# Optimization experiments

Measured on AMD Instinct MI355X. Metric: run time of the kernel, lower is better.

## Reference

```python
import jax, jax.numpy as jnp
import numpy as np

B, N, C, H, W = 16, 10, 128, 48, 48

def setup_inputs() -> dict:
    key = jax.random.key(0)
    k0, k1 = jax.random.split(key, 2)
    x = jax.random.normal(k0, (B, N, C, H, W), dtype=jnp.float32)
    # trainable interpolation params, initialized to 0.5 as in the torch module
    pos_dec = jnp.full((N,), 0.5, dtype=jnp.float32)
    length_dec = jnp.full((N,), 0.5, dtype=jnp.float32)
    # 1x1 conv == channel-mixing matmul over N*C channels
    NC = N * C
    conv_w = jax.random.normal(k1, (NC, NC), dtype=jnp.float32) * (1.0 / np.sqrt(NC))
    conv_b = jnp.zeros((NC,), dtype=jnp.float32)
    return {"x": x, "pos_dec": pos_dec, "length_dec": length_dec,
            "conv_w": conv_w, "conv_b": conv_b}


def reference(x, pos_dec, length_dec, conv_w, conv_b):
    b, n, c, h, w = x.shape
    d = c * h * w
    q = x.reshape(b, n, d)          # proj_query (B,N,CHW)
    k = q                           # proj_key has the same flattened features
    # bi_interpolate with pos_int=i, length_int=1 reduces in closed form to:
    #   s0 = (1-pd)*K[i]   + pd*K[i+1]                      (key_short row)
    #   s1 = ld*((1-pd)*K[i+1] + pd*K[i+2])                 (zero-padded short mixed with key_long)
    # where indices wrap mod N (key was concatenated with itself).
    idx = jnp.arange(n)
    k1_ = k[:, (idx + 1) % n]       # (B,N,D)
    k2_ = k[:, (idx + 2) % n]
    pd = pos_dec[None, :, None]
    ld = length_dec[None, :, None]
    s0 = (1.0 - pd) * k + pd * k1_
    s1 = ld * ((1.0 - pd) * k1_ + pd * k2_)
    S = jnp.stack([s0, s1], axis=2)                 # (B,N,2,D) interpolated keys per group
    logits = jnp.einsum('bnd,bnkd->bnk', q, S)      # per-group 2-way attention scores
    attn = jax.nn.softmax(logits, axis=-1)          # softmax over the 2 searched keys
    out = jnp.einsum('bnk,bnkd->bnd', attn, S)      # (B,N,D)
    feat = out.reshape(b, n * c, h, w)
    conv = jnp.einsum('oc,bchw->bohw', conv_w, feat) + conv_b[None, :, None, None]
    return conv + x.reshape(b, n * c, h, w)
```

## Files before the change

kernel.cpp:

```cpp
#include <hip/hip_runtime.h>
#include <hip/hip_bf16.h>

#define BB 16
#define NN 10
#define CC 128
#define HWD 2304
#define DD (CC*HWD)
#define NC (NN*CC)

#define CH2 72
#define CHUNK2 4096

#define BM 256
#define BN 256
#define BK 64
#define TK (NC/BK)

typedef __bf16 bf16x8 __attribute__((ext_vector_type(8)));
typedef float  f32x4  __attribute__((ext_vector_type(4)));

#define FEAT_BYTES ((size_t)BB*HWD*NC*2)
#define WB_BYTES   ((size_t)NC*NC*2)
#define PART_FLOATS (BB*NN*CH2*3)

__device__ __forceinline__ ushort f2bf(float f) {
    __hip_bfloat16 h = __float2bfloat16(f);
    return *reinterpret_cast<ushort*>(&h);
}

__device__ __forceinline__ void gload_lds16(const ushort* g, ushort* l) {
    __builtin_amdgcn_global_load_lds(
        (const __attribute__((address_space(1))) void*)(const void*)g,
        (__attribute__((address_space(3))) void*)(void*)l,
        16, 0, 0);
}

__global__ __launch_bounds__(256) void k_dots(const float* __restrict__ x,
                                              float* __restrict__ part) {
    int blk = blockIdx.x;
    int ch = blk % CH2;
    int b  = blk / CH2;
    const float* base = x + (size_t)b*NN*DD + (size_t)ch*CHUNK2;
    int t = threadIdx.x;

    float4 cur[4], nxt[4], inc[4];
    #pragma unroll
    for (int i = 0; i < 4; ++i) cur[i] = *(const float4*)(base + (size_t)0*DD + i*1024 + t*4);
    #pragma unroll
    for (int i = 0; i < 4; ++i) nxt[i] = *(const float4*)(base + (size_t)1*DD + i*1024 + t*4);

    __shared__ float red[4][3];
    int w = t >> 6, l = t & 63;

    for (int n = 0; n < NN; ++n) {
        int n2 = (n + 2) % NN;
        #pragma unroll
        for (int i = 0; i < 4; ++i) inc[i] = *(const float4*)(base + (size_t)n2*DD + i*1024 + t*4);

        float s0 = 0.f, s1 = 0.f, s2 = 0.f;
        #pragma unroll
        for (int i = 0; i < 4; ++i) {
            s0 += cur[i].x*cur[i].x + cur[i].y*cur[i].y + cur[i].z*cur[i].z + cur[i].w*cur[i].w;
            s1 += cur[i].x*nxt[i].x + cur[i].y*nxt[i].y + cur[i].z*nxt[i].z + cur[i].w*nxt[i].w;
            s2 += cur[i].x*inc[i].x + cur[i].y*inc[i].y + cur[i].z*inc[i].z + cur[i].w*inc[i].w;
        }
        for (int o = 32; o > 0; o >>= 1) {
            s0 += __shfl_down(s0, o);
            s1 += __shfl_down(s1, o);
            s2 += __shfl_down(s2, o);
        }
        if (l == 0) { red[w][0] = s0; red[w][1] = s1; red[w][2] = s2; }
        __syncthreads();
        if (t == 0) {
            float r0 = 0.f, r1 = 0.f, r2 = 0.f;
            #pragma unroll
            for (int i = 0; i < 4; ++i) { r0 += red[i][0]; r1 += red[i][1]; r2 += red[i][2]; }
            float* o = part + ((size_t)(b*NN + n)*CH2 + ch)*3;
            o[0] = r0; o[1] = r1; o[2] = r2;
        }
        __syncthreads();
        #pragma unroll
        for (int i = 0; i < 4; ++i) { cur[i] = nxt[i]; nxt[i] = inc[i]; }
    }
}

__global__ void k_coef(const float* __restrict__ part,
                       const float* __restrict__ pos_dec,
                       const float* __restrict__ len_dec,
                       float* __restrict__ coef) {
    int bn = threadIdx.x;
    if (bn >= BB*NN) return;
    int n = bn % NN;
    float d0 = 0.f, d1 = 0.f, d2 = 0.f;
    const float* p = part + (size_t)bn*CH2*3;
    for (int i = 0; i < CH2; ++i) { d0 += p[i*3]; d1 += p[i*3+1]; d2 += p[i*3+2]; }
    float pd = pos_dec[n], ld = len_dec[n];
    float l0 = (1.f - pd)*d0 + pd*d1;
    float l1 = ld*((1.f - pd)*d1 + pd*d2);
    float m  = fmaxf(l0, l1);
    float e0 = expf(l0 - m), e1 = expf(l1 - m);
    float inv = 1.f/(e0 + e1);
    float a0 = e0*inv, a1 = e1*inv;
    coef[bn*3+0] = a0*(1.f - pd);
    coef[bn*3+1] = a0*pd + a1*ld*(1.f - pd);
    coef[bn*3+2] = a1*ld*pd;
}

__global__ __launch_bounds__(256) void k_wconv(const float* __restrict__ w,
                                               ushort* __restrict__ wb) {
    int i = blockIdx.x*blockDim.x + threadIdx.x;
    size_t idx = (size_t)i*4;
    if (idx >= (size_t)NC*NC) return;
    float4 a = *(const float4*)(w + idx);
    ushort4 o;
    o.x = f2bf(a.x); o.y = f2bf(a.y); o.z = f2bf(a.z); o.w = f2bf(a.w);
    *(ushort4*)(wb + idx) = o;
}

__global__ __launch_bounds__(256) void k_feat(const float* __restrict__ x,
                                              const float* __restrict__ coef,
                                              ushort* __restrict__ featT) {
    __shared__ float tile[32*129];
    int hwt = blockIdx.x;
    int b   = blockIdx.y;
    int t = threadIdx.x;
    int hw0 = hwt*32;
    const float* xb = x + (size_t)b*NN*DD;

    int c_[4], ch_[4];
    size_t off_[4];
    #pragma unroll
    for (int i = 0; i < 4; ++i) {
        int s = i*256 + t;
        c_[i] = s >> 3; ch_[i] = s & 7;
        off_[i] = (size_t)c_[i]*HWD + hw0 + ch_[i]*4;
    }

    float4 s0[4], s1[4], s2[4], s3[4];
    #pragma unroll
    for (int i = 0; i < 4; ++i) s0[i] = *(const float4*)(xb + (size_t)0*DD + off_[i]);
    #pragma unroll
    for (int i = 0; i < 4; ++i) s1[i] = *(const float4*)(xb + (size_t)1*DD + off_[i]);
    #pragma unroll
    for (int i = 0; i < 4; ++i) s2[i] = *(const float4*)(xb + (size_t)2*DD + off_[i]);

    for (int n = 0; n < NN; ++n) {
        int n3 = (n + 3) % NN;
        #pragma unroll
        for (int i = 0; i < 4; ++i) s3[i] = *(const float4*)(xb + (size_t)n3*DD + off_[i]);

        int bn = b*NN + n;
        float c0 = coef[bn*3+0], c1 = coef[bn*3+1], c2 = coef[bn*3+2];

        #pragma unroll
        for (int i = 0; i < 4; ++i) {
            int hwb = ch_[i]*4, cc = c_[i];
            tile[(hwb+0)*129 + cc] = c0*s0[i].x + c1*s1[i].x + c2*s2[i].x;
            tile[(hwb+1)*129 + cc] = c0*s0[i].y + c1*s1[i].y + c2*s2[i].y;
            tile[(hwb+2)*129 + cc] = c0*s0[i].z + c1*s1[i].z + c2*s2[i].z;
            tile[(hwb+3)*129 + cc] = c0*s0[i].w + c1*s1[i].w + c2*s2[i].w;
        }
        __syncthreads();

        int hwl = t >> 4;
        int cc0 = (t & 15) * 8;
        #pragma unroll
        for (int p = 0; p < 2; ++p) {
            int hw = p*16 + hwl;
            const float* src = &tile[hw*129 + cc0];
            union { ushort us[8]; uint4 v; } pk;
            #pragma unroll
            for (int j = 0; j < 8; ++j) pk.us[j] = f2bf(src[j]);
            ushort* dst = featT + (size_t)b*HWD*NC + (size_t)(hw0 + hw)*NC + n*CC + cc0;
            *(uint4*)dst = pk.v;
        }
        __syncthreads();
        #pragma unroll
        for (int i = 0; i < 4; ++i) { s0[i] = s1[i]; s1[i] = s2[i]; s2[i] = s3[i]; }
    }
}

#define BAR()   __builtin_amdgcn_s_barrier()
#define SB()    __builtin_amdgcn_sched_barrier(0)
#define LGKM0() asm volatile("s_waitcnt lgkmcnt(0)" ::: "memory")
#define VM(N)   asm volatile("s_waitcnt vmcnt(" #N ")" ::: "memory")

__global__ __launch_bounds__(512, 2) void k_gemm(const ushort* __restrict__ Wb,
                                                 const ushort* __restrict__ featT,
                                                 const float* __restrict__ bias,
                                                 const float* __restrict__ x,
                                                 float* __restrict__ out) {
    __shared__ ushort L[2][4][BM*32];

    int bid = blockIdx.x;
    int wkid = (bid & 7) * 90 + (bid >> 3);
    int b   = wkid / 45;
    int r45 = wkid % 45;
    int hwt = r45 / 5;
    int ot  = r45 % 5;
    int o0 = ot*BM, hw0 = hwt*BN;

    int t = threadIdx.x;
    int l = t & 63;
    int w = t >> 6;
    int wr = w >> 2, wc = w & 3;

    const ushort* Ag = Wb + (size_t)o0*NC;
    const ushort* Bg = featT + (size_t)b*HWD*NC + (size_t)hw0*NC;

    int r0 = t >> 2, c0 = t & 3;
    size_t g0 = (size_t)r0*NC + (size_t)((c0 ^ ((r0 >> 1) & 3)) * 8);
    size_t g1 = g0 + (size_t)128*NC;

#define STAGE(nb_, reg_, gp_) do { \
    gload_lds16((gp_) + g0, &L[nb_][reg_][t*8]); \
    gload_lds16((gp_) + g1, &L[nb_][reg_][(512 + t)*8]); } while (0)

    int fr = l & 15;
    int kc = ((l >> 4) ^ ((l >> 1) & 3)) * 8;
    int rowA = (wr*128 + fr)*32 + kc;
    int rowB = (wc*64  + fr)*32 + kc;

    f32x4 acc[8][4] = {};
    bf16x8 af[8], bfA, bfB;

    STAGE(0, 0, Ag);
    STAGE(0, 2, Bg);
    STAGE(0, 1, Ag + 32);
    STAGE(0, 3, Bg + 32);
    VM(4);
    BAR(); SB();

    for (int kt = 0; kt < TK - 1; ++kt) {
        int buf = kt & 1, nbuf = buf ^ 1;
        const ushort* A0 = &L[buf][0][0];
        const ushort* A1 = &L[buf][1][0];
        const ushort* B0 = &L[buf][2][0];
        const ushort* B1 = &L[buf][3][0];
        const ushort* Agk = Ag + (size_t)(kt + 1)*BK;
        const ushort* Bgk = Bg + (size_t)(kt + 1)*BK;

        #pragma unroll
        for (int i = 0; i < 8; ++i) af[i] = *(const bf16x8*)&A0[rowA + i*512];
        bfA = *(const bf16x8*)&B0[rowB];
        bfB = *(const bf16x8*)&B0[rowB + 512];
        STAGE(nbuf, 0, Agk);
        SB(); BAR(); LGKM0(); SB();
        __builtin_amdgcn_s_setprio(1);
        #pragma unroll
        for (int i = 0; i < 8; ++i) {
            acc[i][0] = __builtin_amdgcn_mfma_f32_16x16x32_bf16(af[i], bfA, acc[i][0], 0, 0, 0);
            acc[i][1] = __builtin_amdgcn_mfma_f32_16x16x32_bf16(af[i], bfB, acc[i][1], 0, 0, 0);
        }
        __builtin_amdgcn_s_setprio(0);
        SB(); BAR(); SB();

        bfA = *(const bf16x8*)&B0[rowB + 2*512];
        bfB = *(const bf16x8*)&B0[rowB + 3*512];
        STAGE(nbuf, 2, Bgk);
        SB(); BAR(); LGKM0(); SB();
        __builtin_amdgcn_s_setprio(1);
        #pragma unroll
        for (int i = 0; i < 8; ++i) {
            acc[i][2] = __builtin_amdgcn_mfma_f32_16x16x32_bf16(af[i], bfA, acc[i][2], 0, 0, 0);
            acc[i][3] = __builtin_amdgcn_mfma_f32_16x16x32_bf16(af[i], bfB, acc[i][3], 0, 0, 0);
        }
        __builtin_amdgcn_s_setprio(0);
        SB(); VM(4); BAR(); SB();

        #pragma unroll
        for (int i = 0; i < 8; ++i) af[i] = *(const bf16x8*)&A1[rowA + i*512];
        bfA = *(const bf16x8*)&B1[rowB];
        bfB = *(const bf16x8*)&B1[rowB + 512];
        STAGE(nbuf, 1, Agk + 32);
        SB(); BAR(); LGKM0(); SB();
        __builtin_amdgcn_s_setprio(1);
        #pragma unroll
        for (int i = 0; i < 8; ++i) {
            acc[i][0] = __builtin_amdgcn_mfma_f32_16x16x32_bf16(af[i], bfA, acc[i][0], 0, 0, 0);
            acc[i][1] = __builtin_amdgcn_mfma_f32_16x16x32_bf16(af[i], bfB, acc[i][1], 0, 0, 0);
        }
        __builtin_amdgcn_s_setprio(0);
        SB(); BAR(); SB();

        bfA = *(const bf16x8*)&B1[rowB + 2*512];
        bfB = *(const bf16x8*)&B1[rowB + 3*512];
        STAGE(nbuf, 3, Bgk + 32);
        SB(); BAR(); LGKM0(); SB();
        __builtin_amdgcn_s_setprio(1);
        #pragma unroll
        for (int i = 0; i < 8; ++i) {
            acc[i][2] = __builtin_amdgcn_mfma_f32_16x16x32_bf16(af[i], bfA, acc[i][2], 0, 0, 0);
            acc[i][3] = __builtin_amdgcn_mfma_f32_16x16x32_bf16(af[i], bfB, acc[i][3], 0, 0, 0);
        }
        __builtin_amdgcn_s_setprio(0);
        SB(); VM(4); BAR(); SB();
    }

    {
        const int buf = (TK - 1) & 1;
        const ushort* A0 = &L[buf][0][0];
        const ushort* A1 = &L[buf][1][0];
        const ushort* B0 = &L[buf][2][0];
        const ushort* B1 = &L[buf][3][0];

        #pragma unroll
        for (int i = 0; i < 8; ++i) af[i] = *(const bf16x8*)&A0[rowA + i*512];
        bfA = *(const bf16x8*)&B0[rowB];
        bfB = *(const bf16x8*)&B0[rowB + 512];
        #pragma unroll
        for (int i = 0; i < 8; ++i) {
            acc[i][0] = __builtin_amdgcn_mfma_f32_16x16x32_bf16(af[i], bfA, acc[i][0], 0, 0, 0);
            acc[i][1] = __builtin_amdgcn_mfma_f32_16x16x32_bf16(af[i], bfB, acc[i][1], 0, 0, 0);
        }
        bfA = *(const bf16x8*)&B0[rowB + 2*512];
        bfB = *(const bf16x8*)&B0[rowB + 3*512];
        #pragma unroll
        for (int i = 0; i < 8; ++i) {
            acc[i][2] = __builtin_amdgcn_mfma_f32_16x16x32_bf16(af[i], bfA, acc[i][2], 0, 0, 0);
            acc[i][3] = __builtin_amdgcn_mfma_f32_16x16x32_bf16(af[i], bfB, acc[i][3], 0, 0, 0);
        }
        VM(0);
        BAR(); SB();
        #pragma unroll
        for (int i = 0; i < 8; ++i) af[i] = *(const bf16x8*)&A1[rowA + i*512];
        bfA = *(const bf16x8*)&B1[rowB];
        bfB = *(const bf16x8*)&B1[rowB + 512];
        #pragma unroll
        for (int i = 0; i < 8; ++i) {
            acc[i][0] = __builtin_amdgcn_mfma_f32_16x16x32_bf16(af[i], bfA, acc[i][0], 0, 0, 0);
            acc[i][1] = __builtin_amdgcn_mfma_f32_16x16x32_bf16(af[i], bfB, acc[i][1], 0, 0, 0);
        }
        bfA = *(const bf16x8*)&B1[rowB + 2*512];
        bfB = *(const bf16x8*)&B1[rowB + 3*512];
        #pragma unroll
        for (int i = 0; i < 8; ++i) {
            acc[i][2] = __builtin_amdgcn_mfma_f32_16x16x32_bf16(af[i], bfA, acc[i][2], 0, 0, 0);
            acc[i][3] = __builtin_amdgcn_mfma_f32_16x16x32_bf16(af[i], bfB, acc[i][3], 0, 0, 0);
        }
    }
#undef STAGE

    #pragma unroll
    for (int m = 0; m < 8; ++m) {
        int ro_base = o0 + wr*128 + m*16 + ((l >> 4) << 2);
        #pragma unroll
        for (int n = 0; n < 4; ++n) {
            int col = hw0 + wc*64 + n*16 + (l & 15);
            #pragma unroll
            for (int r = 0; r < 4; ++r) {
                int ro = ro_base + r;
                size_t idx = (size_t)b*NC*HWD + (size_t)ro*HWD + col;
                out[idx] = acc[m][n][r] + bias[ro] + x[idx];
            }
        }
    }
}

extern "C" void kernel_launch(void* const* d_in, const int* in_sizes, int n_in,
                              void* d_out, int out_size, void* d_ws, size_t ws_size,
                              hipStream_t stream) {
    const float* x       = (const float*)d_in[0];
    const float* pos_dec = (const float*)d_in[1];
    const float* len_dec = (const float*)d_in[2];
    const float* conv_w  = (const float*)d_in[3];
    const float* conv_b  = (const float*)d_in[4];
    float* out = (float*)d_out;

    char* ws = (char*)d_ws;
    ushort* featT = (ushort*)ws;
    ushort* wb    = (ushort*)(ws + FEAT_BYTES);
    float*  part  = (float*)(ws + FEAT_BYTES + WB_BYTES);
    float*  coef  = part + PART_FLOATS;

    k_dots <<<dim3(BB*CH2), 256, 0, stream>>>(x, part);
    k_coef <<<dim3(1), 256, 0, stream>>>(part, pos_dec, len_dec, coef);
    k_wconv<<<dim3(1600), 256, 0, stream>>>(conv_w, wb);
    k_feat <<<dim3(72, BB), 256, 0, stream>>>(x, coef, featT);
    k_gemm <<<dim3(720), 512, 0, stream>>>(wb, featT, conv_b, x, out);
}
```

Measured before the change: 300.2 us.

## Fold attention coefficients into per-batch weights and fuse dots with transpose

Rather than building the interpolated feature tensor from x via coefficients, the per-group attention mixing is folded algebraically into a per-batch weight matrix W2[b] = sum of shifted conv_w column blocks scaled by coefficients. The dot-product kernel now also transposes x to bf16 in the same pass, so x is read once for both the dots and the GEMM operand. This removes the separate k_feat pass over x. In exchange it writes a 16x larger weight tensor (per batch, about 52 MB bf16) and requires a large workspace, with a fallback to the old path when the workspace is too small.

Measured after the change: 285.3 us. 1.05x faster.

```diff
diff --git a/kernel.cpp b/kernel.cpp
--- a/kernel.cpp
+++ b/kernel.cpp
@@ -8,8 +8,7 @@
 #define DD (CC*HWD)
 #define NC (NN*CC)
 
-#define CH2 72
-#define CHUNK2 4096
+#define CHP 72
 
 #define BM 256
 #define BN 256
@@ -19,9 +18,11 @@
 typedef __bf16 bf16x8 __attribute__((ext_vector_type(8)));
 typedef float  f32x4  __attribute__((ext_vector_type(4)));
 
-#define FEAT_BYTES ((size_t)BB*HWD*NC*2)
-#define WB_BYTES   ((size_t)NC*NC*2)
-#define PART_FLOATS (BB*NN*CH2*3)
+#define XT_BYTES ((size_t)BB*HWD*NC*2)
+#define W2_BYTES ((size_t)BB*NC*NC*2)
+#define WB_BYTES ((size_t)NC*NC*2)
+#define PART_FLOATS (BB*NN*CHP*3)
+#define HEAD ((size_t)262144)
 
 __device__ __forceinline__ ushort f2bf(float f) {
     __hip_bfloat16 h = __float2bfloat16(f);
@@ -35,52 +36,88 @@
         16, 0, 0);
 }
 
-__global__ __launch_bounds__(256) void k_dots(const float* __restrict__ x,
-                                              float* __restrict__ part) {
-    int blk = blockIdx.x;
-    int ch = blk % CH2;
-    int b  = blk / CH2;
-    const float* base = x + (size_t)b*NN*DD + (size_t)ch*CHUNK2;
+__global__ __launch_bounds__(256) void k_trans(const float* __restrict__ x,
+                                               ushort* __restrict__ xT,
+                                               float* __restrict__ part) {
+    __shared__ float tile[32*129];
+    __shared__ float red[4][3];
+    int hwt = blockIdx.x;
+    int b   = blockIdx.y;
     int t = threadIdx.x;
-
-    float4 cur[4], nxt[4], inc[4];
-    #pragma unroll
-    for (int i = 0; i < 4; ++i) cur[i] = *(const float4*)(base + (size_t)0*DD + i*1024 + t*4);
-    #pragma unroll
-    for (int i = 0; i < 4; ++i) nxt[i] = *(const float4*)(base + (size_t)1*DD + i*1024 + t*4);
-
-    __shared__ float red[4][3];
+    int hw0 = hwt*32;
+    const float* xb = x + (size_t)b*NN*DD;
+
+    int c_[4], ch_[4];
+    size_t off_[4];
+    #pragma unroll
+    for (int i = 0; i < 4; ++i) {
+        int s = i*256 + t;
+        c_[i] = s >> 3; ch_[i] = s & 7;
+        off_[i] = (size_t)c_[i]*HWD + hw0 + ch_[i]*4;
+    }
+
+    float4 s0[4], s1[4], s2[4], s3[4];
+    #pragma unroll
+    for (int i = 0; i < 4; ++i) s0[i] = *(const float4*)(xb + (size_t)0*DD + off_[i]);
+    #pragma unroll
+    for (int i = 0; i < 4; ++i) s1[i] = *(const float4*)(xb + (size_t)1*DD + off_[i]);
+    #pragma unroll
+    for (int i = 0; i < 4; ++i) s2[i] = *(const float4*)(xb + (size_t)2*DD + off_[i]);
+
     int w = t >> 6, l = t & 63;
 
     for (int n = 0; n < NN; ++n) {
-        int n2 = (n + 2) % NN;
-        #pragma unroll
-        for (int i = 0; i < 4; ++i) inc[i] = *(const float4*)(base + (size_t)n2*DD + i*1024 + t*4);
-
-        float s0 = 0.f, s1 = 0.f, s2 = 0.f;
+        int n3 = (n + 3) % NN;
+        #pragma unroll
+        for (int i = 0; i < 4; ++i) s3[i] = *(const float4*)(xb + (size_t)n3*DD + off_[i]);
+
+        float d0 = 0.f, d1 = 0.f, d2 = 0.f;
         #pragma unroll
         for (int i = 0; i < 4; ++i) {
-            s0 += cur[i].x*cur[i].x + cur[i].y*cur[i].y + cur[i].z*cur[i].z + cur[i].w*cur[i].w;
-            s1 += cur[i].x*nxt[i].x + cur[i].y*nxt[i].y + cur[i].z*nxt[i].z + cur[i].w*nxt[i].w;
-            s2 += cur[i].x*inc[i].x + cur[i].y*inc[i].y + cur[i].z*inc[i].z + cur[i].w*inc[i].w;
+            d0 += s0[i].x*s0[i].x + s0[i].y*s0[i].y + s0[i].z*s0[i].z + s0[i].w*s0[i].w;
+            d1 += s0[i].x*s1[i].x + s0[i].y*s1[i].y + s0[i].z*s1[i].z + s0[i].w*s1[i].w;
+            d2 += s0[i].x*s2[i].x + s0[i].y*s2[i].y + s0[i].z*s2[i].z + s0[i].w*s2[i].w;
         }
         for (int o = 32; o > 0; o >>= 1) {
-            s0 += __shfl_down(s0, o);
-            s1 += __shfl_down(s1, o);
-            s2 += __shfl_down(s2, o);
-        }
-        if (l == 0) { red[w][0] = s0; red[w][1] = s1; red[w][2] = s2; }
+            d0 += __shfl_down(d0, o);
+            d1 += __shfl_down(d1, o);
+            d2 += __shfl_down(d2, o);
+        }
+        if (l == 0) { red[w][0] = d0; red[w][1] = d1; red[w][2] = d2; }
+
+        #pragma unroll
+        for (int i = 0; i < 4; ++i) {
+            int hwb = ch_[i]*4, cc = c_[i];
+            tile[(hwb+0)*129 + cc] = s0[i].x;
+            tile[(hwb+1)*129 + cc] = s0[i].y;
+            tile[(hwb+2)*129 + cc] = s0[i].z;
+            tile[(hwb+3)*129 + cc] = s0[i].w;
+        }
         __syncthreads();
+
         if (t == 0) {
             float r0 = 0.f, r1 = 0.f, r2 = 0.f;
             #pragma unroll
             for (int i = 0; i < 4; ++i) { r0 += red[i][0]; r1 += red[i][1]; r2 += red[i][2]; }
-            float* o = part + ((size_t)(b*NN + n)*CH2 + ch)*3;
+            float* o = part + ((size_t)(b*NN + n)*CHP + hwt)*3;
             o[0] = r0; o[1] = r1; o[2] = r2;
         }
+
+        int hwl = t >> 4;
+        int cc0 = (t & 15) * 8;
+        #pragma unroll
+        for (int p = 0; p < 2; ++p) {
+            int hw = p*16 + hwl;
+            const float* src = &tile[hw*129 + cc0];
+            union { ushort us[8]; uint4 v; } pk;
+            #pragma unroll
+            for (int j = 0; j < 8; ++j) pk.us[j] = f2bf(src[j]);
+            ushort* dst = xT + (size_t)b*HWD*NC + (size_t)(hw0 + hw)*NC + n*CC + cc0;
+            *(uint4*)dst = pk.v;
+        }
         __syncthreads();
         #pragma unroll
-        for (int i = 0; i < 4; ++i) { cur[i] = nxt[i]; nxt[i] = inc[i]; }
+        for (int i = 0; i < 4; ++i) { s0[i] = s1[i]; s1[i] = s2[i]; s2[i] = s3[i]; }
     }
 }
 
@@ -92,8 +129,8 @@
     if (bn >= BB*NN) return;
     int n = bn % NN;
     float d0 = 0.f, d1 = 0.f, d2 = 0.f;
-    const float* p = part + (size_t)bn*CH2*3;
-    for (int i = 0; i < CH2; ++i) { d0 += p[i*3]; d1 += p[i*3+1]; d2 += p[i*3+2]; }
+    const float* p = part + (size_t)bn*CHP*3;
+    for (int i = 0; i < CHP; ++i) { d0 += p[i*3]; d1 += p[i*3+1]; d2 += p[i*3+2]; }
     float pd = pos_dec[n], ld = len_dec[n];
     float l0 = (1.f - pd)*d0 + pd*d1;
     float l1 = ld*((1.f - pd)*d1 + pd*d2);
@@ -106,6 +143,37 @@
     coef[bn*3+2] = a1*ld*pd;
 }
 
+__global__ __launch_bounds__(256) void k_w2(const float* __restrict__ w,
+                                            const float* __restrict__ coef,
+                                            ushort* __restrict__ w2) {
+    int b = blockIdx.y;
+    size_t eid = ((size_t)blockIdx.x*256 + threadIdx.x)*8;
+    int o  = (int)(eid / NC);
+    int mc = (int)(eid % NC);
+    int m = mc >> 7, c = mc & 127;
+    int m1 = (m + 9) % 10, m2 = (m + 8) % 10;
+    float c0 = coef[(b*NN + m )*3 + 0];
+    float c1 = coef[(b*NN + m1)*3 + 1];
+    float c2 = coef[(b*NN + m2)*3 + 2];
+    const float* wr = w + (size_t)o*NC;
+    float4 a0 = *(const float4*)(wr + m *128 + c);
+    float4 a1 = *(const float4*)(wr + m *128 + c + 4);
+    float4 u0 = *(const float4*)(wr + m1*128 + c);
+    float4 u1 = *(const float4*)(wr + m1*128 + c + 4);
+    float4 v0 = *(const float4*)(wr + m2*128 + c);
+    float4 v1 = *(const float4*)(wr + m2*128 + c + 4);
+    union { ushort us[8]; uint4 v; } pk;
+    pk.us[0] = f2bf(c0*a0.x + c1*u0.x + c2*v0.x);
+    pk.us[1] = f2bf(c0*a0.y + c1*u0.y + c2*v0.y);
+    pk.us[2] = f2bf(c0*a0.z + c1*u0.z + c2*v0.z);
+    pk.us[3] = f2bf(c0*a0.w + c1*u0.w + c2*v0.w);
+    pk.us[4] = f2bf(c0*a1.x + c1*u1.x + c2*v1.x);
+    pk.us[5] = f2bf(c0*a1.y + c1*u1.y + c2*v1.y);
+    pk.us[6] = f2bf(c0*a1.z + c1*u1.z + c2*v1.z);
+    pk.us[7] = f2bf(c0*a1.w + c1*u1.w + c2*v1.w);
+    *(uint4*)(w2 + (size_t)b*NC*NC + eid) = pk.v;
+}
+
 __global__ __launch_bounds__(256) void k_wconv(const float* __restrict__ w,
                                                ushort* __restrict__ wb) {
     int i = blockIdx.x*blockDim.x + threadIdx.x;
@@ -185,11 +253,12 @@
 #define LGKM0() asm volatile("s_waitcnt lgkmcnt(0)" ::: "memory")
 #define VM(N)   asm volatile("s_waitcnt vmcnt(" #N ")" ::: "memory")
 
-__global__ __launch_bounds__(512, 2) void k_gemm(const ushort* __restrict__ Wb,
-                                                 const ushort* __restrict__ featT,
+__global__ __launch_bounds__(512, 2) void k_gemm(const ushort* __restrict__ Amat,
+                                                 const ushort* __restrict__ Bmat,
                                                  const float* __restrict__ bias,
                                                  const float* __restrict__ x,
-                                                 float* __restrict__ out) {
+                                                 float* __restrict__ out,
+                                                 size_t aStride) {
     __shared__ ushort L[2][4][BM*32];
 
     int bid = blockIdx.x;
@@ -205,8 +274,8 @@
     int w = t >> 6;
     int wr = w >> 2, wc = w & 3;
 
-    const ushort* Ag = Wb + (size_t)o0*NC;
-    const ushort* Bg = featT + (size_t)b*HWD*NC + (size_t)hw0*NC;
+    const ushort* Ag = Amat + (size_t)b*aStride + (size_t)o0*NC;
+    const ushort* Bg = Bmat + (size_t)b*HWD*NC + (size_t)hw0*NC;
 
     int r0 = t >> 2, c0 = t & 3;
     size_t g0 = (size_t)r0*NC + (size_t)((c0 ^ ((r0 >> 1) & 3)) * 8);
@@ -368,14 +437,21 @@
     float* out = (float*)d_out;
 
     char* ws = (char*)d_ws;
-    ushort* featT = (ushort*)ws;
-    ushort* wb    = (ushort*)(ws + FEAT_BYTES);
-    float*  part  = (float*)(ws + FEAT_BYTES + WB_BYTES);
-    float*  coef  = part + PART_FLOATS;
-
-    k_dots <<<dim3(BB*CH2), 256, 0, stream>>>(x, part);
+    float*  part = (float*)ws;
+    float*  coef = part + PART_FLOATS;
+    ushort* xT   = (ushort*)(ws + HEAD);
+
+    k_trans<<<dim3(CHP, BB), 256, 0, stream>>>(x, xT, part);
     k_coef <<<dim3(1), 256, 0, stream>>>(part, pos_dec, len_dec, coef);
-    k_wconv<<<dim3(1600), 256, 0, stream>>>(conv_w, wb);
-    k_feat <<<dim3(72, BB), 256, 0, stream>>>(x, coef, featT);
-    k_gemm <<<dim3(720), 512, 0, stream>>>(wb, featT, conv_b, x, out);
-}
+
+    if (ws_size >= HEAD + XT_BYTES + W2_BYTES) {
+        ushort* w2 = (ushort*)(ws + HEAD + XT_BYTES);
+        k_w2  <<<dim3(800, BB), 256, 0, stream>>>(conv_w, coef, w2);
+        k_gemm<<<dim3(720), 512, 0, stream>>>(w2, xT, conv_b, x, out, (size_t)NC*NC);
+    } else {
+        ushort* wb = (ushort*)(ws + HEAD + XT_BYTES);
+        k_wconv<<<dim3(1600), 256, 0, stream>>>(conv_w, wb);
+        k_feat <<<dim3(CHP, BB), 256, 0, stream>>>(x, coef, xT);
+        k_gemm <<<dim3(720), 512, 0, stream>>>(wb, xT, conv_b, x, out, (size_t)0);
+    }
+}
```
